# Kernel optimization log

Hardware: AMD Instinct MI355X
Metric: run time of the kernel (lower is better)

The kernel has to match this reference:

```python
import jax, jax.numpy as jnp
import numpy as np

DAYS = 10
EPS = 1e-5


def _ln(x, g, b, axis):
    # LayerNorm over a single axis with affine params of shape (x.shape[axis],)
    m = x.mean(axis=axis, keepdims=True)
    v = ((x - m) ** 2).mean(axis=axis, keepdims=True)
    xn = (x - m) * jax.lax.rsqrt(v + EPS)
    shp = [1] * x.ndim
    shp[axis] = x.shape[axis]
    return xn * g.reshape(shp) + b.reshape(shp)


def setup_inputs() -> dict:
    B, T, C = 8192, 30, 64
    H = 30  # lstm hidden
    P = C * (C - 1) // 2  # 2016 pairwise channels
    CH1 = 2 * P + 5 * C + 7 * C  # 4800
    ks = jax.random.split(jax.random.key(0), 16)
    s = 0.05
    x = jax.random.uniform(ks[0], (B, T, C), dtype=jnp.float32, minval=0.5, maxval=1.5)
    inp = {
        'x': x,
        'ln_ts_g': jnp.ones((7, 3), jnp.float32),
        'ln_ts_b': jnp.zeros((7, 3), jnp.float32),
        'pe_w': jax.random.normal(ks[1], (7 * C, C, DAYS), jnp.float32) * s,
        'pe_b': jnp.zeros((7 * C,), jnp.float32),
        'pe_g': jnp.ones((3,), jnp.float32),
        'pe_beta': jnp.zeros((3,), jnp.float32),
        'enc1_w': jax.random.normal(ks[2], (CH1 // 2, CH1), jnp.float32) * s,
        'enc1_b': jnp.zeros((CH1 // 2,), jnp.float32),
        'enc1_g': jnp.ones((3,), jnp.float32),
        'enc1_bb': jnp.zeros((3,), jnp.float32),
        'enc2_w': jax.random.normal(ks[3], (CH1 // 4, CH1 // 2), jnp.float32) * s,
        'enc2_b': jnp.zeros((CH1 // 4,), jnp.float32),
        'enc2_g': jnp.ones((3,), jnp.float32),
        'enc2_bb': jnp.zeros((3,), jnp.float32),
        'enc3_w': jax.random.normal(ks[4], (CH1 // 8, CH1 // 4), jnp.float32) * s,
        'enc3_b': jnp.zeros((CH1 // 8,), jnp.float32),
        'enc3_g': jnp.ones((3,), jnp.float32),
        'enc3_bb': jnp.zeros((3,), jnp.float32),
        'enc4_w': jax.random.normal(ks[5], (CH1 // 16, CH1 // 8), jnp.float32) * s,
        'enc4_b': jnp.zeros((CH1 // 16,), jnp.float32),
        'enc4_g': jnp.ones((3,), jnp.float32),
        'enc4_bb': jnp.zeros((3,), jnp.float32),
        'w_ih': jax.random.normal(ks[6], (4 * H, CH1 // 16), jnp.float32) * s,
        'w_hh': jax.random.normal(ks[7], (4 * H, H), jnp.float32) * s,
        'b_ih': jnp.zeros((4 * H,), jnp.float32),
        'b_hh': jnp.zeros((4 * H,), jnp.float32),
        'ln2_g': jnp.ones((3,), jnp.float32),
        'ln2_b': jnp.zeros((3,), jnp.float32),
        'lin_w': jax.random.normal(ks[8], (1, 3 * H), jnp.float32) * s,
        'lin_b': jnp.zeros((1,), jnp.float32),
    }
    return inp


def reference(x, ln_ts_g, ln_ts_b, pe_w, pe_b, pe_g, pe_beta,
              enc1_w, enc1_b, enc1_g, enc1_bb,
              enc2_w, enc2_b, enc2_g, enc2_bb,
              enc3_w, enc3_b, enc3_g, enc3_bb,
              enc4_w, enc4_b, enc4_g, enc4_bb,
              w_ih, w_hh, b_ih, b_hh, ln2_g, ln2_b, lin_w, lin_b):
    B, T, C = x.shape
    W = T // DAYS  # 3 windows
    xw = x.reshape(B, W, DAYS, C)  # non-overlapping windows (stride == days)
    mu = xw.mean(2)                                    # (B,W,C)  TS_Mean
    xc = xw - mu[:, :, None, :]
    std = jnp.sqrt((xc * xc).sum(2) / (DAYS - 1))      # (B,W,C)  TS_Stddev (unbiased)
    covf = jnp.einsum('bwdi,bwdj->bwij', xc, xc) / (DAYS - 1)
    iu, ju = np.triu_indices(C, 1)
    cov = covf[:, :, iu, ju]                           # (B,W,P)  TS_Cov
    corr = cov / (std[:, :, iu] * std[:, :, ju])       # (B,W,P)  TS_Corr
    zscore = mu / std                                  # TS_Zscore
    ret = xw[:, :, -1, :] / xw[:, :, 0, :] - 1.0       # TS_Return
    dw = jnp.arange(1, DAYS + 1, dtype=x.dtype)
    dw = dw / dw.sum()
    decay = jnp.einsum('bwdc,d->bwc', xw, dw)          # TS_Decaylinear
    branches = [corr, cov, std, zscore, ret, decay, mu]
    # per-branch TS_LayerNorm1d over the time axis (size W=3)
    feats = [_ln(br, ln_ts_g[k], ln_ts_b[k], axis=1) for k, br in enumerate(branches)]
    xfeat = jnp.concatenate(feats, axis=2).transpose(0, 2, 1)  # (B, 2P+5C, W)
    # param_extraction: Conv1d(C, 7C, k=10, s=10) + LayerNorm(W)
    pe = jnp.einsum('bwdc,ocd->bow', xw, pe_w) + pe_b[None, :, None]
    pe = _ln(pe, pe_g, pe_beta, axis=2)                # (B, 7C, W)
    h = jnp.concatenate([xfeat, pe], axis=1)           # (B, ch1, W)
    for w_, b_, g_, bb_ in ((enc1_w, enc1_b, enc1_g, enc1_bb),
                            (enc2_w, enc2_b, enc2_g, enc2_bb),
                            (enc3_w, enc3_b, enc3_g, enc3_bb),
                            (enc4_w, enc4_b, enc4_g, enc4_bb)):
        h = jax.nn.relu(_ln(jnp.einsum('oc,bcw->bow', w_, h) + b_[None, :, None], g_, bb_, axis=2))
    # LSTM over W=3 steps, batch_first
    seq = h.transpose(2, 0, 1)  # (W, B, ch2)
    Hn = w_hh.shape[1]

    def step(carry, xt):
        hp, cp = carry
        gates = xt @ w_ih.T + b_ih + hp @ w_hh.T + b_hh
        i, f, g, o = jnp.split(gates, 4, axis=-1)
        c = jax.nn.sigmoid(f) * cp + jax.nn.sigmoid(i) * jnp.tanh(g)
        hn = jax.nn.sigmoid(o) * jnp.tanh(c)
        return (hn, c), hn

    h0 = jnp.zeros((seq.shape[1], Hn), x.dtype)
    _, ys = jax.lax.scan(step, (h0, h0), seq)          # (W,B,Hn)
    lo = ys.transpose(1, 2, 0)                         # (B,Hn,W)
    lo = _ln(lo, ln2_g, ln2_b, axis=2).reshape(B, -1)  # (B, 3*Hn)
    return lo @ lin_w.T + lin_b                        # (B,1)
```

## Files before the change

### kernel.cpp

```cpp
#include <hip/hip_runtime.h>
#include <cstdint>
#include <cstddef>

#define EPS_LN 1e-5f

constexpr int TB = 30;
constexpr int CC = 64;
constexpr int DD = 10;
constexpr int WN = 3;
constexpr int PP = 2016;
constexpr int F1 = 4352;
constexpr int PEO = 448;
constexpr int CH = 4800;

typedef unsigned short u16;
typedef __attribute__((ext_vector_type(8))) short short8;
typedef __attribute__((ext_vector_type(4))) float f32x4;

__device__ __forceinline__ float sigm(float x) { return 1.f / (1.f + expf(-x)); }

__device__ __forceinline__ u16 f2bf(float v) {
    union { float f; uint32_t u; } c; c.f = v;
    uint32_t u = c.u;
    uint32_t r = (u + 0x7FFFu + ((u >> 16) & 1u)) >> 16;
    return (u16)r;
}
__device__ __forceinline__ float bf2f(u16 h) {
    union { uint32_t u; float f; } c; c.u = ((uint32_t)h) << 16;
    return c.f;
}
__device__ __forceinline__ void store_split(u16* __restrict__ hi, u16* __restrict__ lo,
                                            size_t idx, float v) {
    u16 h = f2bf(v);
    hi[idx] = h;
    lo[idx] = f2bf(v - bf2f(h));
}

__global__ __launch_bounds__(256)
void feat_kernel(const float* __restrict__ x,
                 const float* __restrict__ ln_ts_g, const float* __restrict__ ln_ts_b,
                 const float* __restrict__ pe_w, const float* __restrict__ pe_b,
                 const float* __restrict__ pe_g, const float* __restrict__ pe_beta,
                 u16* __restrict__ hh, u16* __restrict__ hl)
{
    __shared__ float xs[TB * CC];
    __shared__ float mu[WN * CC], sd[WN * CC];
    __shared__ float lg[21], lb[21], pg[3], pb2[3];

    const int tid = threadIdx.x;
    const int b = blockIdx.x;
    const float* xb = x + (size_t)b * (TB * CC);

    for (int i = tid; i < TB * CC; i += 256) xs[i] = xb[i];
    if (tid < 21) { lg[tid] = ln_ts_g[tid]; lb[tid] = ln_ts_b[tid]; }
    if (tid >= 32 && tid < 35) { pg[tid - 32] = pe_g[tid - 32]; pb2[tid - 32] = pe_beta[tid - 32]; }
    __syncthreads();

    if (tid < WN * CC) {
        int w = tid / CC, c = tid % CC;
        float s = 0.f;
#pragma unroll
        for (int d = 0; d < DD; ++d) s += xs[(w * DD + d) * CC + c];
        float m = s * (1.f / DD);
        float q = 0.f;
#pragma unroll
        for (int d = 0; d < DD; ++d) { float t = xs[(w * DD + d) * CC + c] - m; q += t * t; }
        mu[tid] = m;
        sd[tid] = sqrtf(q * (1.f / (DD - 1)));
    }
    __syncthreads();

    const size_t nbase = (size_t)b * WN;

    for (int f = tid; f < F1; f += 256) {
        float v[WN];
        int k;
        if (f < 2 * PP) {
            int p = (f < PP) ? f : (f - PP);
            k = (f < PP) ? 0 : 1;
            int i = (int)((2 * CC - 1 - sqrtf((float)((2 * CC - 1) * (2 * CC - 1) - 8 * p))) * 0.5f);
            if (i < 0) i = 0;
            if (i > CC - 2) i = CC - 2;
            while (((i + 1) * (2 * CC - i - 2)) / 2 <= p) ++i;
            while ((i * (2 * CC - i - 1)) / 2 > p) --i;
            int j = i + 1 + (p - (i * (2 * CC - i - 1)) / 2);
#pragma unroll
            for (int w = 0; w < WN; ++w) {
                float mi = mu[w * CC + i], mj = mu[w * CC + j];
                float s = 0.f;
#pragma unroll
                for (int d = 0; d < DD; ++d)
                    s += (xs[(w * DD + d) * CC + i] - mi) * (xs[(w * DD + d) * CC + j] - mj);
                s *= (1.f / (DD - 1));
                if (k == 0) s /= (sd[w * CC + i] * sd[w * CC + j]);
                v[w] = s;
            }
        } else {
            int r = f - 2 * PP;
            k = 2 + r / CC;
            int c = r % CC;
#pragma unroll
            for (int w = 0; w < WN; ++w) {
                float val;
                if (k == 2) val = sd[w * CC + c];
                else if (k == 3) val = mu[w * CC + c] / sd[w * CC + c];
                else if (k == 4) val = xs[(w * DD + DD - 1) * CC + c] / xs[(w * DD) * CC + c] - 1.f;
                else if (k == 5) {
                    float s = 0.f;
#pragma unroll
                    for (int d = 0; d < DD; ++d) s += xs[(w * DD + d) * CC + c] * (float)(d + 1);
                    val = s * (1.f / 55.f);
                } else val = mu[w * CC + c];
                v[w] = val;
            }
        }
        float m = (v[0] + v[1] + v[2]) * (1.f / 3.f);
        float d0 = v[0] - m, d1 = v[1] - m, d2 = v[2] - m;
        float rs = 1.f / sqrtf((d0 * d0 + d1 * d1 + d2 * d2) * (1.f / 3.f) + EPS_LN);
        store_split(hh, hl, (nbase + 0) * CH + f, d0 * rs * lg[k * 3 + 0] + lb[k * 3 + 0]);
        store_split(hh, hl, (nbase + 1) * CH + f, d1 * rs * lg[k * 3 + 1] + lb[k * 3 + 1]);
        store_split(hh, hl, (nbase + 2) * CH + f, d2 * rs * lg[k * 3 + 2] + lb[k * 3 + 2]);
    }

    for (int o = tid; o < PEO; o += 256) {
        const float* wr = pe_w + (size_t)o * (CC * DD);
        float v0 = 0.f, v1 = 0.f, v2 = 0.f;
        for (int c = 0; c < CC; ++c) {
#pragma unroll
            for (int d = 0; d < DD; ++d) {
                float wv = wr[c * DD + d];
                v0 += xs[(0 * DD + d) * CC + c] * wv;
                v1 += xs[(1 * DD + d) * CC + c] * wv;
                v2 += xs[(2 * DD + d) * CC + c] * wv;
            }
        }
        float bo = pe_b[o];
        v0 += bo; v1 += bo; v2 += bo;
        float m = (v0 + v1 + v2) * (1.f / 3.f);
        float d0 = v0 - m, d1 = v1 - m, d2 = v2 - m;
        float rs = 1.f / sqrtf((d0 * d0 + d1 * d1 + d2 * d2) * (1.f / 3.f) + EPS_LN);
        store_split(hh, hl, (nbase + 0) * CH + F1 + o, d0 * rs * pg[0] + pb2[0]);
        store_split(hh, hl, (nbase + 1) * CH + F1 + o, d1 * rs * pg[1] + pb2[1]);
        store_split(hh, hl, (nbase + 2) * CH + F1 + o, d2 * rs * pg[2] + pb2[2]);
    }
}

__global__ __launch_bounds__(256)
void wconv_ker(const float* __restrict__ W, int O, int K, int Kpad,
               u16* __restrict__ Wh, u16* __restrict__ Wl)
{
    int idx = blockIdx.x * 256 + threadIdx.x;
    if (idx >= O * Kpad) return;
    int o = idx / Kpad, k = idx - o * Kpad;
    float v = (k < K) ? W[(size_t)o * K + k] : 0.f;
    u16 h = f2bf(v);
    Wh[idx] = h;
    Wl[idx] = f2bf(v - bf2f(h));
}

template<int BO, int BN>
__global__ __launch_bounds__(256)
void gemm_mfma(const u16* __restrict__ Whi, const u16* __restrict__ Wlo,
               const u16* __restrict__ Xhi, const u16* __restrict__ Xlo,
               const float* __restrict__ bias, float* __restrict__ Y,
               int O, int Kpad, int N)
{
    constexpr int LDW = 40;
    __shared__ u16 Ah[BN][LDW], Al[BN][LDW], Bh[BO][LDW], Bl[BO][LDW];

    const int tid = threadIdx.x;
    const int o0 = blockIdx.x * BO;
    const int n0 = blockIdx.y * BN;

    const int w  = tid >> 6;
    const int wn = w >> 1, wo = w & 1;
    const int l  = tid & 63;
    const int lr = l & 15, lhi = l >> 4;

    const int sr = tid >> 2;
    const int sq = tid & 3;

    f32x4 acc[4][4];
#pragma unroll
    for (int m = 0; m < 4; ++m)
#pragma unroll
        for (int n = 0; n < 4; ++n) acc[m][n] = (f32x4)0.f;

    for (int k0 = 0; k0 < Kpad; k0 += 32) {
#pragma unroll
        for (int rep = 0; rep < BN / 64; ++rep) {
            int row = rep * 64 + sr;
            const size_t g = (size_t)(n0 + row) * Kpad + k0 + sq * 8;
            *reinterpret_cast<int4*>(&Ah[row][sq * 8]) = *reinterpret_cast<const int4*>(Xhi + g);
            *reinterpret_cast<int4*>(&Al[row][sq * 8]) = *reinterpret_cast<const int4*>(Xlo + g);
        }
#pragma unroll
        for (int rep = 0; rep < BO / 64; ++rep) {
            int row = rep * 64 + sr;
            int orow = o0 + row;
            int4 vh = make_int4(0, 0, 0, 0), vl = make_int4(0, 0, 0, 0);
            if (orow < O) {
                const size_t g = (size_t)orow * Kpad + k0 + sq * 8;
                vh = *reinterpret_cast<const int4*>(Whi + g);
                vl = *reinterpret_cast<const int4*>(Wlo + g);
            }
            *reinterpret_cast<int4*>(&Bh[row][sq * 8]) = vh;
            *reinterpret_cast<int4*>(&Bl[row][sq * 8]) = vl;
        }
        __syncthreads();

        short8 ah[4], al[4], bh[4], bl[4];
#pragma unroll
        for (int m = 0; m < 4; ++m) {
            int row = wn * 64 + m * 16 + lr;
            ah[m] = *reinterpret_cast<const short8*>(&Ah[row][lhi * 8]);
            al[m] = *reinterpret_cast<const short8*>(&Al[row][lhi * 8]);
        }
#pragma unroll
        for (int n = 0; n < 4; ++n) {
            int row = wo * 64 + n * 16 + lr;
            bh[n] = *reinterpret_cast<const short8*>(&Bh[row][lhi * 8]);
            bl[n] = *reinterpret_cast<const short8*>(&Bl[row][lhi * 8]);
        }
#pragma unroll
        for (int m = 0; m < 4; ++m)
#pragma unroll
            for (int n = 0; n < 4; ++n) {
                acc[m][n] = __builtin_amdgcn_mfma_f32_16x16x32_bf16(ah[m], bh[n], acc[m][n], 0, 0, 0);
                acc[m][n] = __builtin_amdgcn_mfma_f32_16x16x32_bf16(ah[m], bl[n], acc[m][n], 0, 0, 0);
                acc[m][n] = __builtin_amdgcn_mfma_f32_16x16x32_bf16(al[m], bh[n], acc[m][n], 0, 0, 0);
            }
        __syncthreads();
    }

#pragma unroll
    for (int n = 0; n < 4; ++n) {
        int o = o0 + wo * 64 + n * 16 + lr;
        if (o >= O) continue;
        float bv = bias[o];
#pragma unroll
        for (int m = 0; m < 4; ++m) {
            int nrow = n0 + wn * 64 + m * 16 + lhi * 4;
#pragma unroll
            for (int r = 0; r < 4; ++r)
                Y[(size_t)(nrow + r) * O + o] = acc[m][n][r] + bv;
        }
    }
}

__global__ __launch_bounds__(256)
void ln_relu_bf16(const float* __restrict__ Y, const float* __restrict__ g,
                  const float* __restrict__ bb, int O, int Opad, int Bc,
                  u16* __restrict__ Xh, u16* __restrict__ Xl)
{
    int idx = blockIdx.x * 256 + threadIdx.x;
    if (idx >= Bc * Opad) return;
    int b = idx / Opad, o = idx - b * Opad;
    size_t ob = (size_t)b * 3 * Opad + o;
    if (o >= O) {
        Xh[ob] = 0; Xl[ob] = 0;
        Xh[ob + Opad] = 0; Xl[ob + Opad] = 0;
        Xh[ob + 2 * (size_t)Opad] = 0; Xl[ob + 2 * (size_t)Opad] = 0;
        return;
    }
    const float* p = Y + (size_t)b * 3 * O + o;
    float y0 = p[0], y1 = p[(size_t)O], y2 = p[(size_t)2 * O];
    float m = (y0 + y1 + y2) * (1.f / 3.f);
    float d0 = y0 - m, d1 = y1 - m, d2 = y2 - m;
    float rs = 1.f / sqrtf((d0 * d0 + d1 * d1 + d2 * d2) * (1.f / 3.f) + EPS_LN);
    store_split(Xh, Xl, ob,                     fmaxf(d0 * rs * g[0] + bb[0], 0.f));
    store_split(Xh, Xl, ob + Opad,              fmaxf(d1 * rs * g[1] + bb[1], 0.f));
    store_split(Xh, Xl, ob + 2 * (size_t)Opad,  fmaxf(d2 * rs * g[2] + bb[2], 0.f));
}

__global__ __launch_bounds__(256)
void lstm_ker(const float* __restrict__ gates,
              const float* __restrict__ w_hh, const float* __restrict__ b_hh,
              const float* __restrict__ ln2g, const float* __restrict__ ln2b,
              const float* __restrict__ lin_w, const float* __restrict__ lin_b,
              float* __restrict__ out, int Bc)
{
    __shared__ float whh[120 * 30];
    __shared__ float bhh[120];
    __shared__ float lw[90];
    __shared__ float lg[3], lbv[3];
    __shared__ float hbuf[8][32];

    const int tid = threadIdx.x;
    for (int i = tid; i < 3600; i += 256) whh[i] = w_hh[i];
    if (tid < 120) bhh[tid] = b_hh[tid];
    if (tid < 90) lw[tid] = lin_w[tid];
    if (tid < 3) { lg[tid] = ln2g[tid]; lbv[tid] = ln2b[tid]; }

    const int g = tid >> 5;
    const int u = tid & 31;
    const int bl = blockIdx.x * 8 + g;

    hbuf[g][u] = 0.f;
    __syncthreads();

    float cstate = 0.f;
    float y0 = 0.f, y1 = 0.f, y2 = 0.f;

#pragma unroll
    for (int t = 0; t < 3; ++t) {
        float hn = 0.f;
        if (u < 30) {
            const float* gr = gates + (size_t)(bl * 3 + t) * 120;
            float gi = gr[u]      + bhh[u];
            float gf = gr[30 + u] + bhh[30 + u];
            float gg = gr[60 + u] + bhh[60 + u];
            float go = gr[90 + u] + bhh[90 + u];
            for (int v = 0; v < 30; ++v) {
                float hv = hbuf[g][v];
                gi += whh[u * 30 + v] * hv;
                gf += whh[(30 + u) * 30 + v] * hv;
                gg += whh[(60 + u) * 30 + v] * hv;
                go += whh[(90 + u) * 30 + v] * hv;
            }
            float cn = sigm(gf) * cstate + sigm(gi) * tanhf(gg);
            cstate = cn;
            hn = sigm(go) * tanhf(cn);
        }
        __syncthreads();
        if (u < 30) hbuf[g][u] = hn;
        __syncthreads();
        if (t == 0) y0 = hn; else if (t == 1) y1 = hn; else y2 = hn;
    }

    float acc = 0.f;
    if (u < 30) {
        float m = (y0 + y1 + y2) * (1.f / 3.f);
        float d0 = y0 - m, d1 = y1 - m, d2 = y2 - m;
        float rs = 1.f / sqrtf((d0 * d0 + d1 * d1 + d2 * d2) * (1.f / 3.f) + EPS_LN);
        acc  = (d0 * rs * lg[0] + lbv[0]) * lw[u * 3 + 0];
        acc += (d1 * rs * lg[1] + lbv[1]) * lw[u * 3 + 1];
        acc += (d2 * rs * lg[2] + lbv[2]) * lw[u * 3 + 2];
    }
#pragma unroll
    for (int off = 16; off > 0; off >>= 1)
        acc += __shfl_down(acc, off, 32);
    if (u == 0) out[bl] = acc + lin_b[0];
}

extern "C" void kernel_launch(void* const* d_in, const int* in_sizes, int n_in,
                              void* d_out, int out_size, void* d_ws, size_t ws_size,
                              hipStream_t stream)
{
    const float* x       = (const float*)d_in[0];
    const float* ln_ts_g = (const float*)d_in[1];
    const float* ln_ts_b = (const float*)d_in[2];
    const float* pe_w    = (const float*)d_in[3];
    const float* pe_b    = (const float*)d_in[4];
    const float* pe_g    = (const float*)d_in[5];
    const float* pe_beta = (const float*)d_in[6];
    const float* e1w = (const float*)d_in[7];  const float* e1b  = (const float*)d_in[8];
    const float* e1g = (const float*)d_in[9];  const float* e1bb = (const float*)d_in[10];
    const float* e2w = (const float*)d_in[11]; const float* e2b  = (const float*)d_in[12];
    const float* e2g = (const float*)d_in[13]; const float* e2bb = (const float*)d_in[14];
    const float* e3w = (const float*)d_in[15]; const float* e3b  = (const float*)d_in[16];
    const float* e3g = (const float*)d_in[17]; const float* e3bb = (const float*)d_in[18];
    const float* e4w = (const float*)d_in[19]; const float* e4b  = (const float*)d_in[20];
    const float* e4g = (const float*)d_in[21]; const float* e4bb = (const float*)d_in[22];
    const float* w_ih = (const float*)d_in[23];
    const float* w_hh = (const float*)d_in[24];
    const float* b_ih = (const float*)d_in[25];
    const float* b_hh = (const float*)d_in[26];
    const float* ln2g = (const float*)d_in[27];
    const float* ln2b = (const float*)d_in[28];
    const float* lin_w = (const float*)d_in[29];
    const float* lin_b = (const float*)d_in[30];
    float* out = (float*)d_out;

    const int Btot = 8192;

    const int LO[5]  = {2400, 1200, 600, 300, 120};
    const int LK[5]  = {4800, 2400, 1200, 600, 300};
    const int LKP[5] = {4800, 2400, 1216, 608, 320};
    const float* LW[5] = {e1w, e2w, e3w, e4w, w_ih};

    u16* wp = (u16*)d_ws;
    u16* Wh[5]; u16* Wl[5];
    size_t wcount = 0;
    for (int i = 0; i < 5; ++i) {
        Wh[i] = wp + wcount; wcount += (size_t)LO[i] * LKP[i];
        Wl[i] = wp + wcount; wcount += (size_t)LO[i] * LKP[i];
    }
    const size_t wbytes = wcount * sizeof(u16);

    const size_t per_b = (size_t)3 * 4800 * 2 * 2 + (size_t)3 * 2400 * 2 * 2 + (size_t)3 * 2400 * 4;
    int Bc = 2048;
    while (Bc > 128 && wbytes + (size_t)Bc * per_b > ws_size) Bc >>= 1;
    const int n_chunks = Btot / Bc;
    const int N = Bc * 3;

    u16* Xah = wp + wcount;            wcount += (size_t)N * 4800;
    u16* Xal = wp + wcount;            wcount += (size_t)N * 4800;
    u16* Xbh = wp + wcount;            wcount += (size_t)N * 2400;
    u16* Xbl = wp + wcount;            wcount += (size_t)N * 2400;
    float* Yf = (float*)(wp + wcount);

    for (int i = 0; i < 5; ++i) {
        int tot = LO[i] * LKP[i];
        wconv_ker<<<(tot + 255) / 256, 256, 0, stream>>>(LW[i], LO[i], LK[i], LKP[i], Wh[i], Wl[i]);
    }

    for (int c = 0; c < n_chunks; ++c) {
        const int b0 = c * Bc;
        feat_kernel<<<Bc, 256, 0, stream>>>(x + (size_t)b0 * TB * CC,
                                            ln_ts_g, ln_ts_b, pe_w, pe_b, pe_g, pe_beta,
                                            Xah, Xal);

        gemm_mfma<128, 128><<<dim3((2400 + 127) / 128, N / 128), 256, 0, stream>>>(
            Wh[0], Wl[0], Xah, Xal, e1b, Yf, 2400, 4800, N);
        ln_relu_bf16<<<(Bc * 2400 + 255) / 256, 256, 0, stream>>>(Yf, e1g, e1bb, 2400, 2400, Bc, Xbh, Xbl);

        gemm_mfma<128, 128><<<dim3((1200 + 127) / 128, N / 128), 256, 0, stream>>>(
            Wh[1], Wl[1], Xbh, Xbl, e2b, Yf, 1200, 2400, N);
        ln_relu_bf16<<<(Bc * 1216 + 255) / 256, 256, 0, stream>>>(Yf, e2g, e2bb, 1200, 1216, Bc, Xah, Xal);

        gemm_mfma<128, 128><<<dim3((600 + 127) / 128, N / 128), 256, 0, stream>>>(
            Wh[2], Wl[2], Xah, Xal, e3b, Yf, 600, 1216, N);
        ln_relu_bf16<<<(Bc * 608 + 255) / 256, 256, 0, stream>>>(Yf, e3g, e3bb, 600, 608, Bc, Xbh, Xbl);

        gemm_mfma<128, 128><<<dim3((300 + 127) / 128, N / 128), 256, 0, stream>>>(
            Wh[3], Wl[3], Xbh, Xbl, e4b, Yf, 300, 608, N);
        ln_relu_bf16<<<(Bc * 320 + 255) / 256, 256, 0, stream>>>(Yf, e4g, e4bb, 300, 320, Bc, Xah, Xal);

        gemm_mfma<128, 128><<<dim3(1, N / 128), 256, 0, stream>>>(
            Wh[4], Wl[4], Xah, Xal, b_ih, Yf, 120, 320, N);

        lstm_ker<<<Bc / 8, 256, 0, stream>>>(Yf, w_hh, b_hh, ln2g, ln2b,
                                             lin_w, lin_b, out + b0, Bc);
    }
}
```

Measured before the change: 6.352 ms.

## Fuse window LayerNorm+ReLU into GEMM epilogue with async LDS loads

Each encoder GEMM now applies bias, the 3-window LayerNorm, ReLU and the hi/lo bf16 split in its epilogue. To make that possible, N tiles are 126 rows wide so each tile holds whole triplets, and the fp32 intermediate round trip plus the separate ln_relu kernels are removed. Operand staging moves to global_load_lds direct-to-LDS loads into an XOR-swizzled 64-wide layout that packs hi and lo halves together. The feature kernel is also split so each pair's covariance is computed once for both the correlation and covariance outputs. The trade-offs are wasted tile rows, padded buffers and extra syncs in the epilogue.

New measurement: 5.759 ms. 9.3% less time.

```diff
diff --git a/kernel.cpp b/kernel.cpp
--- a/kernel.cpp
+++ b/kernel.cpp
@@ -34,6 +34,11 @@
     u16 h = f2bf(v);
     hi[idx] = h;
     lo[idx] = f2bf(v - bf2f(h));
+}
+
+__device__ __forceinline__ void gll16(const void* g, void* l) {
+    __builtin_amdgcn_global_load_lds((const __attribute__((address_space(1))) void*)g,
+                                     (__attribute__((address_space(3))) void*)l, 16, 0, 0);
 }
 
 __global__ __launch_bounds__(256)
@@ -72,54 +77,57 @@
 
     const size_t nbase = (size_t)b * WN;
 
-    for (int f = tid; f < F1; f += 256) {
-        float v[WN];
-        int k;
-        if (f < 2 * PP) {
-            int p = (f < PP) ? f : (f - PP);
-            k = (f < PP) ? 0 : 1;
-            int i = (int)((2 * CC - 1 - sqrtf((float)((2 * CC - 1) * (2 * CC - 1) - 8 * p))) * 0.5f);
-            if (i < 0) i = 0;
-            if (i > CC - 2) i = CC - 2;
-            while (((i + 1) * (2 * CC - i - 2)) / 2 <= p) ++i;
-            while ((i * (2 * CC - i - 1)) / 2 > p) --i;
-            int j = i + 1 + (p - (i * (2 * CC - i - 1)) / 2);
-#pragma unroll
-            for (int w = 0; w < WN; ++w) {
-                float mi = mu[w * CC + i], mj = mu[w * CC + j];
+    auto ln3store = [&](float v0, float v1, float v2, int k, int col) {
+        float m = (v0 + v1 + v2) * (1.f / 3.f);
+        float d0 = v0 - m, d1 = v1 - m, d2 = v2 - m;
+        float rs = 1.f / sqrtf((d0 * d0 + d1 * d1 + d2 * d2) * (1.f / 3.f) + EPS_LN);
+        store_split(hh, hl, (nbase + 0) * CH + col, d0 * rs * lg[k * 3 + 0] + lb[k * 3 + 0]);
+        store_split(hh, hl, (nbase + 1) * CH + col, d1 * rs * lg[k * 3 + 1] + lb[k * 3 + 1]);
+        store_split(hh, hl, (nbase + 2) * CH + col, d2 * rs * lg[k * 3 + 2] + lb[k * 3 + 2]);
+    };
+
+    for (int p = tid; p < PP; p += 256) {
+        int i = (int)((2 * CC - 1 - sqrtf((float)((2 * CC - 1) * (2 * CC - 1) - 8 * p))) * 0.5f);
+        if (i < 0) i = 0;
+        if (i > CC - 2) i = CC - 2;
+        while (((i + 1) * (2 * CC - i - 2)) / 2 <= p) ++i;
+        while ((i * (2 * CC - i - 1)) / 2 > p) --i;
+        int j = i + 1 + (p - (i * (2 * CC - i - 1)) / 2);
+        float cv[3], cr[3];
+#pragma unroll
+        for (int w = 0; w < WN; ++w) {
+            float mi = mu[w * CC + i], mj = mu[w * CC + j];
+            float s = 0.f;
+#pragma unroll
+            for (int d = 0; d < DD; ++d)
+                s += (xs[(w * DD + d) * CC + i] - mi) * (xs[(w * DD + d) * CC + j] - mj);
+            s *= (1.f / (DD - 1));
+            cv[w] = s;
+            cr[w] = s / (sd[w * CC + i] * sd[w * CC + j]);
+        }
+        ln3store(cr[0], cr[1], cr[2], 0, p);
+        ln3store(cv[0], cv[1], cv[2], 1, PP + p);
+    }
+
+    for (int f = tid; f < 5 * CC; f += 256) {
+        int k = 2 + f / CC;
+        int c = f % CC;
+        float v[3];
+#pragma unroll
+        for (int w = 0; w < WN; ++w) {
+            float val;
+            if (k == 2) val = sd[w * CC + c];
+            else if (k == 3) val = mu[w * CC + c] / sd[w * CC + c];
+            else if (k == 4) val = xs[(w * DD + DD - 1) * CC + c] / xs[(w * DD) * CC + c] - 1.f;
+            else if (k == 5) {
                 float s = 0.f;
 #pragma unroll
-                for (int d = 0; d < DD; ++d)
-                    s += (xs[(w * DD + d) * CC + i] - mi) * (xs[(w * DD + d) * CC + j] - mj);
-                s *= (1.f / (DD - 1));
-                if (k == 0) s /= (sd[w * CC + i] * sd[w * CC + j]);
-                v[w] = s;
-            }
-        } else {
-            int r = f - 2 * PP;
-            k = 2 + r / CC;
-            int c = r % CC;
-#pragma unroll
-            for (int w = 0; w < WN; ++w) {
-                float val;
-                if (k == 2) val = sd[w * CC + c];
-                else if (k == 3) val = mu[w * CC + c] / sd[w * CC + c];
-                else if (k == 4) val = xs[(w * DD + DD - 1) * CC + c] / xs[(w * DD) * CC + c] - 1.f;
-                else if (k == 5) {
-                    float s = 0.f;
-#pragma unroll
-                    for (int d = 0; d < DD; ++d) s += xs[(w * DD + d) * CC + c] * (float)(d + 1);
-                    val = s * (1.f / 55.f);
-                } else val = mu[w * CC + c];
-                v[w] = val;
-            }
-        }
-        float m = (v[0] + v[1] + v[2]) * (1.f / 3.f);
-        float d0 = v[0] - m, d1 = v[1] - m, d2 = v[2] - m;
-        float rs = 1.f / sqrtf((d0 * d0 + d1 * d1 + d2 * d2) * (1.f / 3.f) + EPS_LN);
-        store_split(hh, hl, (nbase + 0) * CH + f, d0 * rs * lg[k * 3 + 0] + lb[k * 3 + 0]);
-        store_split(hh, hl, (nbase + 1) * CH + f, d1 * rs * lg[k * 3 + 1] + lb[k * 3 + 1]);
-        store_split(hh, hl, (nbase + 2) * CH + f, d2 * rs * lg[k * 3 + 2] + lb[k * 3 + 2]);
+                for (int d = 0; d < DD; ++d) s += xs[(w * DD + d) * CC + c] * (float)(d + 1);
+                val = s * (1.f / 55.f);
+            } else val = mu[w * CC + c];
+            v[w] = val;
+        }
+        ln3store(v[0], v[1], v[2], k, 2 * PP + f);
     }
 
     for (int o = tid; o < PEO; o += 256) {
@@ -158,27 +166,33 @@
     Wl[idx] = f2bf(v - bf2f(h));
 }
 
-template<int BO, int BN>
+template<bool FUSE>
 __global__ __launch_bounds__(256)
 void gemm_mfma(const u16* __restrict__ Whi, const u16* __restrict__ Wlo,
                const u16* __restrict__ Xhi, const u16* __restrict__ Xlo,
-               const float* __restrict__ bias, float* __restrict__ Y,
-               int O, int Kpad, int N)
+               const float* __restrict__ bias,
+               const float* __restrict__ lng, const float* __restrict__ lnb,
+               int O, int Kpad, int N, int Ntrip, int Opad,
+               u16* __restrict__ Oh, u16* __restrict__ Ol,
+               float* __restrict__ Yf)
 {
-    constexpr int LDW = 40;
-    __shared__ u16 Ah[BN][LDW], Al[BN][LDW], Bh[BO][LDW], Bl[BO][LDW];
+    union SMem {
+        struct { u16 A[128 * 64]; u16 B[128 * 64]; } s;
+        float L[128][68];
+    };
+    __shared__ SMem sm;
 
     const int tid = threadIdx.x;
-    const int o0 = blockIdx.x * BO;
-    const int n0 = blockIdx.y * BN;
+    const int o0 = blockIdx.x * 128;
+    const int n0 = blockIdx.y * 126;
+    const int T0 = blockIdx.y * 42;
 
     const int w  = tid >> 6;
     const int wn = w >> 1, wo = w & 1;
     const int l  = tid & 63;
     const int lr = l & 15, lhi = l >> 4;
-
-    const int sr = tid >> 2;
-    const int sq = tid & 3;
+    const int rg = l >> 3, sl = l & 7;
+    const int ck = sl ^ rg;
 
     f32x4 acc[4][4];
 #pragma unroll
@@ -188,39 +202,38 @@
 
     for (int k0 = 0; k0 < Kpad; k0 += 32) {
 #pragma unroll
-        for (int rep = 0; rep < BN / 64; ++rep) {
-            int row = rep * 64 + sr;
-            const size_t g = (size_t)(n0 + row) * Kpad + k0 + sq * 8;
-            *reinterpret_cast<int4*>(&Ah[row][sq * 8]) = *reinterpret_cast<const int4*>(Xhi + g);
-            *reinterpret_cast<int4*>(&Al[row][sq * 8]) = *reinterpret_cast<const int4*>(Xlo + g);
-        }
-#pragma unroll
-        for (int rep = 0; rep < BO / 64; ++rep) {
-            int row = rep * 64 + sr;
-            int orow = o0 + row;
-            int4 vh = make_int4(0, 0, 0, 0), vl = make_int4(0, 0, 0, 0);
-            if (orow < O) {
-                const size_t g = (size_t)orow * Kpad + k0 + sq * 8;
-                vh = *reinterpret_cast<const int4*>(Whi + g);
-                vl = *reinterpret_cast<const int4*>(Wlo + g);
-            }
-            *reinterpret_cast<int4*>(&Bh[row][sq * 8]) = vh;
-            *reinterpret_cast<int4*>(&Bl[row][sq * 8]) = vl;
+        for (int j = 0; j < 8; ++j) {
+            int blk = j * 4 + w;
+            if (blk < 16) {
+                int row = blk * 8 + rg;
+                size_t gb = (size_t)(n0 + row) * Kpad + k0;
+                const u16* src = (ck < 4) ? (Xhi + gb + ck * 8) : (Xlo + gb + (ck - 4) * 8);
+                gll16(src, &sm.s.A[blk * 512]);
+            } else {
+                int row = (blk - 16) * 8 + rg;
+                size_t gb = (size_t)(o0 + row) * Kpad + k0;
+                const u16* src = (ck < 4) ? (Whi + gb + ck * 8) : (Wlo + gb + (ck - 4) * 8);
+                gll16(src, &sm.s.B[(blk - 16) * 512]);
+            }
         }
         __syncthreads();
 
         short8 ah[4], al[4], bh[4], bl[4];
 #pragma unroll
         for (int m = 0; m < 4; ++m) {
-            int row = wn * 64 + m * 16 + lr;
-            ah[m] = *reinterpret_cast<const short8*>(&Ah[row][lhi * 8]);
-            al[m] = *reinterpret_cast<const short8*>(&Al[row][lhi * 8]);
+            int r = wn * 64 + m * 16 + lr;
+            int shi = lhi ^ (r & 7);
+            int slo = (4 ^ lhi) ^ (r & 7);
+            ah[m] = *reinterpret_cast<const short8*>(&sm.s.A[r * 64 + shi * 8]);
+            al[m] = *reinterpret_cast<const short8*>(&sm.s.A[r * 64 + slo * 8]);
         }
 #pragma unroll
         for (int n = 0; n < 4; ++n) {
-            int row = wo * 64 + n * 16 + lr;
-            bh[n] = *reinterpret_cast<const short8*>(&Bh[row][lhi * 8]);
-            bl[n] = *reinterpret_cast<const short8*>(&Bl[row][lhi * 8]);
+            int r = wo * 64 + n * 16 + lr;
+            int shi = lhi ^ (r & 7);
+            int slo = (4 ^ lhi) ^ (r & 7);
+            bh[n] = *reinterpret_cast<const short8*>(&sm.s.B[r * 64 + shi * 8]);
+            bl[n] = *reinterpret_cast<const short8*>(&sm.s.B[r * 64 + slo * 8]);
         }
 #pragma unroll
         for (int m = 0; m < 4; ++m)
@@ -233,44 +246,71 @@
         __syncthreads();
     }
 
-#pragma unroll
-    for (int n = 0; n < 4; ++n) {
-        int o = o0 + wo * 64 + n * 16 + lr;
-        if (o >= O) continue;
-        float bv = bias[o];
-#pragma unroll
-        for (int m = 0; m < 4; ++m) {
-            int nrow = n0 + wn * 64 + m * 16 + lhi * 4;
-#pragma unroll
-            for (int r = 0; r < 4; ++r)
-                Y[(size_t)(nrow + r) * O + o] = acc[m][n][r] + bv;
-        }
-    }
-}
-
-__global__ __launch_bounds__(256)
-void ln_relu_bf16(const float* __restrict__ Y, const float* __restrict__ g,
-                  const float* __restrict__ bb, int O, int Opad, int Bc,
-                  u16* __restrict__ Xh, u16* __restrict__ Xl)
-{
-    int idx = blockIdx.x * 256 + threadIdx.x;
-    if (idx >= Bc * Opad) return;
-    int b = idx / Opad, o = idx - b * Opad;
-    size_t ob = (size_t)b * 3 * Opad + o;
-    if (o >= O) {
-        Xh[ob] = 0; Xl[ob] = 0;
-        Xh[ob + Opad] = 0; Xl[ob + Opad] = 0;
-        Xh[ob + 2 * (size_t)Opad] = 0; Xl[ob + 2 * (size_t)Opad] = 0;
-        return;
-    }
-    const float* p = Y + (size_t)b * 3 * O + o;
-    float y0 = p[0], y1 = p[(size_t)O], y2 = p[(size_t)2 * O];
-    float m = (y0 + y1 + y2) * (1.f / 3.f);
-    float d0 = y0 - m, d1 = y1 - m, d2 = y2 - m;
-    float rs = 1.f / sqrtf((d0 * d0 + d1 * d1 + d2 * d2) * (1.f / 3.f) + EPS_LN);
-    store_split(Xh, Xl, ob,                     fmaxf(d0 * rs * g[0] + bb[0], 0.f));
-    store_split(Xh, Xl, ob + Opad,              fmaxf(d1 * rs * g[1] + bb[1], 0.f));
-    store_split(Xh, Xl, ob + 2 * (size_t)Opad,  fmaxf(d2 * rs * g[2] + bb[2], 0.f));
+    float bv[4];
+#pragma unroll
+    for (int nf = 0; nf < 4; ++nf) {
+        int o = o0 + wo * 64 + nf * 16 + lr;
+        bv[nf] = (o < O) ? bias[o] : 0.f;
+    }
+
+    if constexpr (!FUSE) {
+#pragma unroll
+        for (int nf = 0; nf < 4; ++nf) {
+            int o = o0 + wo * 64 + nf * 16 + lr;
+            if (o >= O) continue;
+#pragma unroll
+            for (int m = 0; m < 4; ++m) {
+                int nb = n0 + wn * 64 + m * 16 + lhi * 4;
+#pragma unroll
+                for (int r = 0; r < 4; ++r) {
+                    int n = nb + r;
+                    if (n < N) Yf[(size_t)n * O + o] = acc[m][nf][r] + bv[nf];
+                }
+            }
+        }
+    } else {
+        const float g0 = lng[0], g1 = lng[1], g2 = lng[2];
+        const float q0 = lnb[0], q1 = lnb[1], q2 = lnb[2];
+        for (int h = 0; h < 2; ++h) {
+            __syncthreads();
+            if (wo == h) {
+#pragma unroll
+                for (int m = 0; m < 4; ++m)
+#pragma unroll
+                    for (int nf = 0; nf < 4; ++nf)
+#pragma unroll
+                        for (int r = 0; r < 4; ++r)
+                            sm.L[wn * 64 + m * 16 + lhi * 4 + r][nf * 16 + lr] = acc[m][nf][r] + bv[nf];
+            }
+            __syncthreads();
+            for (int it = 0; it < 11; ++it) {
+                int item = it * 256 + tid;
+                if (item < 42 * 64) {
+                    int tl = item >> 6, c2 = item & 63;
+                    int t = T0 + tl;
+                    int o = o0 + h * 64 + c2;
+                    if (t < Ntrip && o < Opad) {
+                        size_t base = (size_t)(3 * t) * Opad + o;
+                        if (o >= O) {
+                            Oh[base] = 0; Ol[base] = 0;
+                            Oh[base + Opad] = 0; Ol[base + Opad] = 0;
+                            Oh[base + 2 * (size_t)Opad] = 0; Ol[base + 2 * (size_t)Opad] = 0;
+                        } else {
+                            float y0 = sm.L[3 * tl + 0][c2];
+                            float y1 = sm.L[3 * tl + 1][c2];
+                            float y2 = sm.L[3 * tl + 2][c2];
+                            float mm = (y0 + y1 + y2) * (1.f / 3.f);
+                            float d0 = y0 - mm, d1 = y1 - mm, d2 = y2 - mm;
+                            float rs = 1.f / sqrtf((d0 * d0 + d1 * d1 + d2 * d2) * (1.f / 3.f) + EPS_LN);
+                            store_split(Oh, Ol, base,                    fmaxf(d0 * rs * g0 + q0, 0.f));
+                            store_split(Oh, Ol, base + Opad,             fmaxf(d1 * rs * g1 + q1, 0.f));
+                            store_split(Oh, Ol, base + 2 * (size_t)Opad, fmaxf(d2 * rs * g2 + q2, 0.f));
+                        }
+                    }
+                }
+            }
+        }
+    }
 }
 
 __global__ __launch_bounds__(256)
@@ -388,22 +428,25 @@
     }
     const size_t wbytes = wcount * sizeof(u16);
 
-    const size_t per_b = (size_t)3 * 4800 * 2 * 2 + (size_t)3 * 2400 * 2 * 2 + (size_t)3 * 2400 * 4;
+    const size_t per_b = (size_t)3 * 4800 * 2 * 2 + (size_t)3 * 2400 * 2 * 2 + (size_t)3 * 128 * 4;
+    const size_t slack = (size_t)128 * (4800 + 2400) * 2 * 2 + 4096;
     int Bc = 2048;
-    while (Bc > 128 && wbytes + (size_t)Bc * per_b > ws_size) Bc >>= 1;
+    while (Bc > 128 && wbytes + slack + (size_t)Bc * per_b > ws_size) Bc >>= 1;
     const int n_chunks = Btot / Bc;
     const int N = Bc * 3;
 
-    u16* Xah = wp + wcount;            wcount += (size_t)N * 4800;
-    u16* Xal = wp + wcount;            wcount += (size_t)N * 4800;
-    u16* Xbh = wp + wcount;            wcount += (size_t)N * 2400;
-    u16* Xbl = wp + wcount;            wcount += (size_t)N * 2400;
+    u16* Xah = wp + wcount;            wcount += (size_t)(N + 128) * 4800;
+    u16* Xal = wp + wcount;            wcount += (size_t)(N + 128) * 4800;
+    u16* Xbh = wp + wcount;            wcount += (size_t)(N + 128) * 2400;
+    u16* Xbl = wp + wcount;            wcount += (size_t)(N + 128) * 2400;
     float* Yf = (float*)(wp + wcount);
 
     for (int i = 0; i < 5; ++i) {
         int tot = LO[i] * LKP[i];
         wconv_ker<<<(tot + 255) / 256, 256, 0, stream>>>(LW[i], LO[i], LK[i], LKP[i], Wh[i], Wl[i]);
     }
+
+    const int GY = (N + 125) / 126;
 
     for (int c = 0; c < n_chunks; ++c) {
         const int b0 = c * Bc;
@@ -411,24 +454,25 @@
                                             ln_ts_g, ln_ts_b, pe_w, pe_b, pe_g, pe_beta,
                                             Xah, Xal);
 
-        gemm_mfma<128, 128><<<dim3((2400 + 127) / 128, N / 128), 256, 0, stream>>>(
-            Wh[0], Wl[0], Xah, Xal, e1b, Yf, 2400, 4800, N);
-        ln_relu_bf16<<<(Bc * 2400 + 255) / 256, 256, 0, stream>>>(Yf, e1g, e1bb, 2400, 2400, Bc, Xbh, Xbl);
-
-        gemm_mfma<128, 128><<<dim3((1200 + 127) / 128, N / 128), 256, 0, stream>>>(
-            Wh[1], Wl[1], Xbh, Xbl, e2b, Yf, 1200, 2400, N);
-        ln_relu_bf16<<<(Bc * 1216 + 255) / 256, 256, 0, stream>>>(Yf, e2g, e2bb, 1200, 1216, Bc, Xah, Xal);
-
-        gemm_mfma<128, 128><<<dim3((600 + 127) / 128, N / 128), 256, 0, stream>>>(
-            Wh[2], Wl[2], Xah, Xal, e3b, Yf, 600, 1216, N);
-        ln_relu_bf16<<<(Bc * 608 + 255) / 256, 256, 0, stream>>>(Yf, e3g, e3bb, 600, 608, Bc, Xbh, Xbl);
-
-        gemm_mfma<128, 128><<<dim3((300 + 127) / 128, N / 128), 256, 0, stream>>>(
-            Wh[3], Wl[3], Xbh, Xbl, e4b, Yf, 300, 608, N);
-        ln_relu_bf16<<<(Bc * 320 + 255) / 256, 256, 0, stream>>>(Yf, e4g, e4bb, 300, 320, Bc, Xah, Xal);
-
-        gemm_mfma<128, 128><<<dim3(1, N / 128), 256, 0, stream>>>(
-            Wh[4], Wl[4], Xah, Xal, b_ih, Yf, 120, 320, N);
+        gemm_mfma<true><<<dim3(19, GY), 256, 0, stream>>>(
+            Wh[0], Wl[0], Xah, Xal, e1b, e1g, e1bb,
+            2400, 4800, N, Bc, 2400, Xbh, Xbl, nullptr);
+
+        gemm_mfma<true><<<dim3(10, GY), 256, 0, stream>>>(
+            Wh[1], Wl[1], Xbh, Xbl, e2b, e2g, e2bb,
+            1200, 2400, N, Bc, 1216, Xah, Xal, nullptr);
+
+        gemm_mfma<true><<<dim3(5, GY), 256, 0, stream>>>(
+            Wh[2], Wl[2], Xah, Xal, e3b, e3g, e3bb,
+            600, 1216, N, Bc, 608, Xbh, Xbl, nullptr);
+
+        gemm_mfma<true><<<dim3(3, GY), 256, 0, stream>>>(
+            Wh[3], Wl[3], Xbh, Xbl, e4b, e4g, e4bb,
+            300, 608, N, Bc, 320, Xah, Xal, nullptr);
+
+        gemm_mfma<false><<<dim3(1, GY), 256, 0, stream>>>(
+            Wh[4], Wl[4], Xah, Xal, b_ih, nullptr, nullptr,
+            120, 320, N, Bc, 120, nullptr, nullptr, Yf);
 
         lstm_ker<<<Bc / 8, 256, 0, stream>>>(Yf, w_hh, b_hh, ln2g, ln2b,
                                              lin_w, lin_b, out + b0, Bc);
```
